# Performance work log

Hardware: AMD Instinct MI355X
Metric: run time of the kernel (lower is better)

Reference implementation:

```python
import math
import jax, jax.numpy as jnp
import numpy as np

L, NH, DF = 4, 4, 32  # num_layers, num_heads, head_dim (H=128)
EPS = 1e-5


def ln(x, g, b):
    m = x.mean(-1, keepdims=True)
    v = ((x - m) ** 2).mean(-1, keepdims=True)
    return (x - m) * jax.lax.rsqrt(v + EPS) * g + b


def mha(x, w_in, b_in, w_out, b_out):
    # torch nn.MultiheadAttention self-attention, batch_first, no mask
    B, S, H = x.shape
    q, k, v = jnp.split(x @ w_in + b_in, 3, axis=-1)
    q = q.reshape(B, S, NH, DF)
    k = k.reshape(B, S, NH, DF)
    v = v.reshape(B, S, NH, DF)
    s = jnp.einsum('bqhd,bkhd->bhqk', q, k) / math.sqrt(DF)
    a = jax.nn.softmax(s, axis=-1)
    o = jnp.einsum('bhqk,bkhd->bqhd', a, v).reshape(B, S, H)
    return o @ w_out + b_out


def _forward(X_k, time_embed, step_embed, W_tr, b_tr, W_in, b_in, g_in, be_in,
             W_e, b_e, aw, ab, ow, ob, tng, tnb, f1w, f1b, f2w, f2b, fng, fnb,
             Wq, Wk, Wv, Wo, bo, Wem, bem, Wea, bea, e1w, e1b, e2w, e2b,
             gng, gnb, eng, enb, W_out, b_out, k_index, edge_index):
    B, N, T1, Cin = X_k.shape
    H = W_in.shape[1]
    # --- precompute_graph: self-loops + structural edge features ---
    loop = jnp.arange(N, dtype=edge_index.dtype)
    ei = jnp.concatenate([edge_index, jnp.stack([loop, loop])], axis=1)
    dst, src = ei[0], ei[1]
    E = ei.shape[1]
    deg = jnp.zeros((N,), jnp.float32).at[dst].add(1.0)
    deg_max = jnp.maximum(deg.max(), 1.0)
    edge_w = 1.0 / jnp.maximum(deg[dst], 1.0)
    feat = jnp.stack([edge_w, deg[src] / deg_max, deg[dst] / deg_max], axis=1)  # [E,3]
    # --- input embedding ---
    t_emb = time_embed  # [T1, te] (lookup of arange(T1) = whole table)
    X = jnp.concatenate(
        [X_k, jnp.broadcast_to(t_emb[None, None], (B, N, T1, t_emb.shape[-1]))], axis=-1)
    h = ln(X @ W_in + b_in, g_in, be_in)
    h = h + step_embed[k_index][:, None, None, :]
    e = feat @ W_e + b_e                       # [E, de]
    t_re = t_emb @ W_tr + b_tr                 # [T1, H]
    BT = B * T1
    for l in range(L):
        # temporal attention over T1
        h_flat = h.reshape(B * N, T1, H)
        attn_out = mha(h_flat, aw[l], ab[l], ow[l], ob[l])
        h = ln(h + attn_out.reshape(B, N, T1, H), tng[l], tnb[l])
        ffn = jax.nn.gelu(h @ f1w[l] + f1b[l], approximate=False) @ f2w[l] + f2b[l]
        h = ln(h + ffn, fng[l], fnb[l])
        h = h + t_re[None, None]
        # DiGress GT sparse graph block over N
        h_BT = h.transpose(0, 2, 1, 3).reshape(BT, N, H)
        Q = (h_BT @ Wq[l]).reshape(BT, N, NH, DF)
        K = (h_BT @ Wk[l]).reshape(BT, N, NH, DF)
        V = (h_BT @ Wv[l]).reshape(BT, N, NH, DF)
        scores = (Q[:, dst] * K[:, src]).sum(-1) / math.sqrt(DF)  # [BT,E,NH]
        scores = scores * (e @ Wem[l] + bem[l] + 1.0) + (e @ Wea[l] + bea[l])
        s_max = jax.lax.stop_gradient(scores.max(axis=1, keepdims=True))
        exp_s = jnp.exp(scores - s_max)
        denom = jnp.zeros((BT, N, NH), exp_s.dtype).at[:, dst, :].add(exp_s)
        attn = exp_s / (denom[:, dst, :] + 1e-9)
        agg = (attn[..., None] * V[:, src]).reshape(BT, E, H)
        out = jnp.zeros((BT, N, H), h.dtype).at[:, dst, :].add(agg)
        h_BT = h_BT + out @ Wo[l] + bo[l]
        h_mean = jax.lax.stop_gradient(h_BT).mean(0)               # [N,H]
        e_in = jnp.concatenate([h_mean[dst], h_mean[src], e], axis=-1)
        e_mlp = jax.nn.gelu(e_in @ e1w[l] + e1b[l], approximate=False) @ e2w[l] + e2b[l]
        e = ln(e + e_mlp, eng[l], enb[l])
        h = ln(h_BT.reshape(B, T1, N, H).transpose(0, 2, 1, 3), gng[l], gnb[l])
    return jax.nn.softmax(h @ W_out + b_out, axis=-1)


def setup_inputs() -> dict:
    key = jax.random.key(0)
    B, N, T1 = 2, 2000, 12
    sd, cc, te, H, de, nh = 4, 2, 16, 128, 16, 4
    Cin = (1 + cc) * sd  # 12
    E0, max_steps = 32000, 1024
    ks = iter(jax.random.split(key, 60))
    def rn(*shape, s=0.05):
        return jax.random.normal(next(ks), shape, jnp.float32) * s
    z = lambda *s: jnp.zeros(s, jnp.float32)
    o = lambda *s: jnp.ones(s, jnp.float32)
    return dict(
        X_k=jax.random.normal(next(ks), (B, N, T1, Cin), jnp.float32),
        time_embed=rn(T1, te), step_embed=rn(max_steps, H),
        W_tr=rn(te, H), b_tr=z(H),
        W_in=rn(Cin + te, H), b_in=z(H), g_in=o(H), be_in=z(H),
        W_e=rn(3, de), b_e=z(de),
        aw=rn(L, H, 3 * H), ab=z(L, 3 * H), ow=rn(L, H, H), ob=z(L, H),
        tng=o(L, H), tnb=z(L, H),
        f1w=rn(L, H, 2 * H), f1b=z(L, 2 * H), f2w=rn(L, 2 * H, H), f2b=z(L, H),
        fng=o(L, H), fnb=z(L, H),
        Wq=rn(L, H, H), Wk=rn(L, H, H), Wv=rn(L, H, H),
        Wo=rn(L, H, H), bo=z(L, H),
        Wem=rn(L, de, nh), bem=z(L, nh), Wea=rn(L, de, nh), bea=z(L, nh),
        e1w=rn(L, 2 * H + de, 4 * de), e1b=z(L, 4 * de),
        e2w=rn(L, 4 * de, de), e2b=z(L, de),
        gng=o(L, H), gnb=z(L, H), eng=o(L, de), enb=z(L, de),
        W_out=rn(H, sd), b_out=z(sd),
        k_index=jax.random.randint(next(ks), (B,), 0, max_steps),
        edge_index=jax.random.randint(next(ks), (2, E0), 0, N),
    )


def reference(X_k, time_embed, step_embed, W_tr, b_tr, W_in, b_in, g_in, be_in,
              W_e, b_e, aw, ab, ow, ob, tng, tnb, f1w, f1b, f2w, f2b, fng, fnb,
              Wq, Wk, Wv, Wo, bo, Wem, bem, Wea, bea, e1w, e1b, e2w, e2b,
              gng, gnb, eng, enb, W_out, b_out, k_index, edge_index):
    return _forward(X_k, time_embed, step_embed, W_tr, b_tr, W_in, b_in, g_in, be_in,
                    W_e, b_e, aw, ab, ow, ob, tng, tnb, f1w, f1b, f2w, f2b, fng, fnb,
                    Wq, Wk, Wv, Wo, bo, Wem, bem, Wea, bea, e1w, e1b, e2w, e2b,
                    gng, gnb, eng, enb, W_out, b_out, k_index, edge_index)
```

## Files before the change

kernel.cpp:

```cpp
#include <hip/hip_runtime.h>
#include <math.h>

#define NN 2000
#define T1C 12
#define BBC 2
#define HHC 128
#define NHD 4
#define DFD 32
#define LLC 4
#define DEC 16
#define TEC 16
#define CINC 12
#define E0C 32000
#define EEC 34000
#define BTC 24
#define MROWS 48000
#define EPSLN 1e-5f
#define SCALEQK 0.17677669529663687f

typedef __attribute__((ext_vector_type(8))) short short8;
typedef __attribute__((ext_vector_type(4))) float f32x4;


__device__ __forceinline__ unsigned short f2b(float f)
{
    unsigned u = __float_as_uint(f);
    return (unsigned short)((u + 0x7FFF + ((u >> 16) & 1)) >> 16);
}

__device__ __forceinline__ float b2f(unsigned short h)
{
    return __uint_as_float(((unsigned)h) << 16);
}


__global__ __launch_bounds__(256) void convwp_k(const float* __restrict__ W, unsigned short* __restrict__ Bp,
                                                int LN_, int K, int N, int noff, int Ntot)
{
    int idx = blockIdx.x * blockDim.x + threadIdx.x;
    int total = LN_ * K * N;
    if (idx >= total) return;
    int l = idx / (K * N);
    int r = idx - l * (K * N);
    int k = r / N;
    int n = r - k * N + noff;
    size_t off = (size_t)l * K * Ntot +
                 ((size_t)((n >> 4) * (K >> 5) + (k >> 5)) << 9) +
                 (((k >> 3) & 3) << 7) + ((n & 15) << 3) + (k & 7);
    Bp[off] = f2b(W[idx]);
}

__global__ __launch_bounds__(256) void convw12_k(const float* __restrict__ e1w, unsigned short* __restrict__ W12P)
{
    int idx = blockIdx.x * blockDim.x + threadIdx.x;
    if (idx >= LLC * 128 * 128) return;
    int l = idx >> 14;
    int r = idx & 16383;
    int c = r >> 7, k = r & 127;
    int sk = (c < 64) ? k : k + 128;
    int sc = c & 63;
    W12P[idx] = f2b(e1w[((size_t)l * 272 + sk) * 64 + sc]);
}

__global__ __launch_bounds__(256) void convwoT_k(const float* __restrict__ Wo, unsigned short* __restrict__ WoT)
{
    int idx = blockIdx.x * blockDim.x + threadIdx.x;
    if (idx >= LLC * 128 * 128) return;
    int l = idx >> 14;
    int r = idx & 16383;
    int c = r >> 7, k = r & 127;
    WoT[idx] = f2b(Wo[((size_t)l * 128 + k) * 128 + c]);
}


template<int K, int EPI, int OUTM>
__global__ __launch_bounds__(256) void gemm2_k(
    const unsigned short* __restrict__ A, const unsigned short* __restrict__ Bp,
    const float* __restrict__ bias, float* __restrict__ C, unsigned short* __restrict__ Cb,
    const float* __restrict__ res, const float* __restrict__ gam, const float* __restrict__ bet,
    const float* __restrict__ trep,
    int M, int Ntot)
{
    __shared__ unsigned short A_s[128 * 16 * 8];
    __shared__ float red2[2][128][2];

    int tid = threadIdx.x;
    int w = tid >> 6, lane = tid & 63;
    int wr = w & 1, wc = w >> 1;
    int quad = lane >> 4, lr = lane & 15;

    const unsigned short* abase = A + (size_t)blockIdx.x * 128 * K;
    int ntg0 = blockIdx.y * 8 + wc * 4;

    f32x4 acc[4][4];
#pragma unroll
    for (int mt = 0; mt < 4; mt++)
#pragma unroll
        for (int nt = 0; nt < 4; nt++) acc[mt][nt] = (f32x4){0.f, 0.f, 0.f, 0.f};

#pragma unroll
    for (int kb = 0; kb < K; kb += 128) {
        if (kb) __syncthreads();
#pragma unroll
        for (int j = 0; j < 8; j++) {
            int s = j * 256 + tid;
            int row = s >> 4, ks = s & 15;
            int ko = ks ^ (row & 15);
            uint4 d = *(const uint4*)(abase + (size_t)row * K + kb + ko * 8);
            *(uint4*)(A_s + s * 8) = d;
        }
        __syncthreads();
#pragma unroll
        for (int k0 = 0; k0 < 128; k0 += 32) {
            short8 af[4], bf[4];
#pragma unroll
            for (int mt = 0; mt < 4; mt++) {
                int row_l = wr * 64 + mt * 16 + lr;
                int koct = (k0 >> 3) + quad;
                int slot = row_l * 16 + (koct ^ lr);
                af[mt] = *(const short8*)(A_s + slot * 8);
            }
#pragma unroll
            for (int nt = 0; nt < 4; nt++) {
                size_t off = ((size_t)(ntg0 + nt) * (K >> 5) + ((kb + k0) >> 5)) * 512 + lane * 8;
                bf[nt] = *(const short8*)(Bp + off);
            }
#pragma unroll
            for (int mt = 0; mt < 4; mt++)
#pragma unroll
                for (int nt = 0; nt < 4; nt++)
                    acc[mt][nt] = __builtin_amdgcn_mfma_f32_16x16x32_bf16(af[mt], bf[nt], acc[mt][nt], 0, 0, 0);
        }
    }

    int rbase = blockIdx.x * 128 + wr * 64;
    int cbase = blockIdx.y * 128 + wc * 64;

    if constexpr (EPI != 3 && EPI != 4 && EPI != 5) {
#pragma unroll
        for (int mt = 0; mt < 4; mt++) {
#pragma unroll
            for (int nt = 0; nt < 4; nt++) {
                int colg = cbase + nt * 16 + lr;
                float bv = bias ? bias[colg] : 0.f;
#pragma unroll
                for (int i = 0; i < 4; i++) {
                    int row = rbase + mt * 16 + quad * 4 + i;
                    float x = acc[mt][nt][i] + bv;
                    if constexpr (EPI == 1) x = 0.5f * x * (1.f + erff(x * 0.70710678118654752f));
                    if constexpr (EPI == 2) x = res[(size_t)row * Ntot + colg] + x;
                    if constexpr (OUTM & 1) C[(size_t)row * Ntot + colg] = x;
                    if constexpr (OUTM & 4)
                        Cb[(size_t)blockIdx.y * M * 128 + (size_t)row * 128 + (wc * 64 + nt * 16 + lr)] = f2b(x);
                    else if constexpr (OUTM & 2)
                        Cb[(size_t)row * Ntot + colg] = f2b(x);
                }
            }
        }
    } else {
        float s[4][4], s2l[4][4];
#pragma unroll
        for (int mt = 0; mt < 4; mt++)
#pragma unroll
            for (int i = 0; i < 4; i++) { s[mt][i] = 0.f; s2l[mt][i] = 0.f; }
#pragma unroll
        for (int mt = 0; mt < 4; mt++) {
#pragma unroll
            for (int nt = 0; nt < 4; nt++) {
                int colg = cbase + nt * 16 + lr;
                float bv = bias[colg];
#pragma unroll
                for (int i = 0; i < 4; i++) {
                    int row = rbase + mt * 16 + quad * 4 + i;
                    float x = acc[mt][nt][i] + bv + res[(size_t)row * 128 + colg];
                    acc[mt][nt][i] = x;
                    s[mt][i] += x;
                    s2l[mt][i] += x * x;
                }
            }
        }
#pragma unroll
        for (int m = 1; m < 16; m <<= 1) {
#pragma unroll
            for (int mt = 0; mt < 4; mt++)
#pragma unroll
                for (int i = 0; i < 4; i++) {
                    s[mt][i]  += __shfl_xor(s[mt][i], m, 64);
                    s2l[mt][i] += __shfl_xor(s2l[mt][i], m, 64);
                }
        }
        if (lr == 0) {
#pragma unroll
            for (int mt = 0; mt < 4; mt++)
#pragma unroll
                for (int i = 0; i < 4; i++) {
                    int rl = wr * 64 + mt * 16 + quad * 4 + i;
                    red2[wc][rl][0] = s[mt][i];
                    red2[wc][rl][1] = s2l[mt][i];
                }
        }
        __syncthreads();
#pragma unroll
        for (int mt = 0; mt < 4; mt++) {
#pragma unroll
            for (int i = 0; i < 4; i++) {
                int rl = wr * 64 + mt * 16 + quad * 4 + i;
                float st  = red2[0][rl][0] + red2[1][rl][0];
                float s2t = red2[0][rl][1] + red2[1][rl][1];
                float mu = st * (1.f / 128.f);
                float rstd = rsqrtf(s2t * (1.f / 128.f) - mu * mu + EPSLN);
                int row = rbase + mt * 16 + quad * 4 + i;
                if constexpr (EPI == 4) {
                    int t = row % T1C;
                    int bn = row / T1C;
                    int b = bn / NN;
                    int n = bn - b * NN;
                    size_t rowp = (size_t)(b * T1C + t) * NN + n;
                    const float* trow = trep + t * HHC;
#pragma unroll
                    for (int nt = 0; nt < 4; nt++) {
                        int colg = cbase + nt * 16 + lr;
                        float y = (acc[mt][nt][i] - mu) * rstd * gam[colg] + bet[colg] + trow[colg];
                        C[rowp * 128 + colg] = y;
                        Cb[rowp * 128 + colg] = f2b(y);
                    }
                } else if constexpr (EPI == 5) {
                    int bt = row / NN, n = row - bt * NN;
                    int b = bt / T1C, t = bt - b * T1C;
                    size_t rowp = ((size_t)(b * NN + n)) * T1C + t;
#pragma unroll
                    for (int nt = 0; nt < 4; nt++) {
                        int colg = cbase + nt * 16 + lr;
                        float y = (acc[mt][nt][i] - mu) * rstd * gam[colg] + bet[colg];
                        C[rowp * 128 + colg] = y;
                        Cb[rowp * 128 + colg] = f2b(y);
                    }
                } else {
#pragma unroll
                    for (int nt = 0; nt < 4; nt++) {
                        int colg = cbase + nt * 16 + lr;
                        float y = (acc[mt][nt][i] - mu) * rstd * gam[colg] + bet[colg];
                        if constexpr (OUTM & 1) C[(size_t)row * 128 + colg] = y;
                        if constexpr (OUTM & 2) Cb[(size_t)row * 128 + colg] = f2b(y);
                    }
                }
            }
        }
    }
}

template<int K, int EPI, int OUTM>
static void run_gemm2(const unsigned short* A, const unsigned short* Bp, const float* bias,
                      float* C, unsigned short* Cb, const float* res, const float* g, const float* be,
                      const float* trep, int M, int Ntot, hipStream_t stream)
{
    dim3 grid(M / 128, Ntot / 128);
    gemm2_k<K, EPI, OUTM><<<grid, 256, 0, stream>>>(A, Bp, bias, C, Cb, res, g, be, trep, M, Ntot);
}


__global__ __launch_bounds__(256) void offn_k(
    const unsigned short* __restrict__ A,
    const unsigned short* __restrict__ Wp,
    const float* __restrict__ ob_l,
    const float* __restrict__ resh,
    const float* __restrict__ tng_l, const float* __restrict__ tnb_l,
    const unsigned short* __restrict__ F1p,
    const unsigned short* __restrict__ F2p,
    const float* __restrict__ f1b_l, const float* __restrict__ f2b_l,
    const float* __restrict__ fng_l, const float* __restrict__ fnb_l,
    const float* __restrict__ trep,
    const unsigned short* __restrict__ Wqkv,
    float* __restrict__ C,
    unsigned short* __restrict__ Qc, unsigned short* __restrict__ Kc, unsigned short* __restrict__ Vc)
{
    __shared__ unsigned short A_s[32 * 16 * 8];
    __shared__ unsigned short M_s[32 * 16 * 8];
    __shared__ float red2[2][32][2];

    int tid = threadIdx.x;
    int w = tid >> 6, lane = tid & 63;
    int wr = w & 1, wc = w >> 1;
    int quad = lane >> 4, lr = lane & 15;

    const unsigned short* abase = A + (size_t)blockIdx.x * 32 * 128;

#pragma unroll
    for (int j = 0; j < 2; j++) {
        int s = j * 256 + tid;
        int row = s >> 4, ks = s & 15;
        int ko = ks ^ (row & 15);
        uint4 d = *(const uint4*)(abase + (size_t)row * 128 + ko * 8);
        *(uint4*)(A_s + s * 8) = d;
    }
    __syncthreads();

    f32x4 wacc[4];
#pragma unroll
    for (int nt = 0; nt < 4; nt++) wacc[nt] = (f32x4){0.f, 0.f, 0.f, 0.f};
#pragma unroll
    for (int k0 = 0; k0 < 128; k0 += 32) {
        int row_l = wr * 16 + lr;
        int koct = (k0 >> 3) + quad;
        int slot = row_l * 16 + (koct ^ lr);
        short8 af = *(const short8*)(A_s + slot * 8);
        short8 bf[4];
#pragma unroll
        for (int nt = 0; nt < 4; nt++) {
            size_t off = ((size_t)(wc * 4 + nt) * 4 + (k0 >> 5)) * 512 + lane * 8;
            bf[nt] = *(const short8*)(Wp + off);
        }
#pragma unroll
        for (int nt = 0; nt < 4; nt++)
            wacc[nt] = __builtin_amdgcn_mfma_f32_16x16x32_bf16(af, bf[nt], wacc[nt], 0, 0, 0);
    }

    int rbase = blockIdx.x * 32 + wr * 16;
    int cbase = wc * 64;

    float yv[4][4];
    {
        float s1[4], s2v[4];
#pragma unroll
        for (int i = 0; i < 4; i++) { s1[i] = 0.f; s2v[i] = 0.f; }
#pragma unroll
        for (int nt = 0; nt < 4; nt++) {
            int colg = cbase + nt * 16 + lr;
            float bv = ob_l[colg];
#pragma unroll
            for (int i = 0; i < 4; i++) {
                int row = rbase + quad * 4 + i;
                float x = wacc[nt][i] + bv + resh[(size_t)row * 128 + colg];
                yv[nt][i] = x;
                s1[i] += x;
                s2v[i] += x * x;
            }
        }
#pragma unroll
        for (int m = 1; m < 16; m <<= 1) {
#pragma unroll
            for (int i = 0; i < 4; i++) {
                s1[i]  += __shfl_xor(s1[i], m, 64);
                s2v[i] += __shfl_xor(s2v[i], m, 64);
            }
        }
        if (lr == 0) {
#pragma unroll
            for (int i = 0; i < 4; i++) {
                int rl = wr * 16 + quad * 4 + i;
                red2[wc][rl][0] = s1[i];
                red2[wc][rl][1] = s2v[i];
            }
        }
        __syncthreads();
#pragma unroll
        for (int i = 0; i < 4; i++) {
            int rl = wr * 16 + quad * 4 + i;
            float st  = red2[0][rl][0] + red2[1][rl][0];
            float s2t = red2[0][rl][1] + red2[1][rl][1];
            float mu = st * (1.f / 128.f);
            float rstd = rsqrtf(s2t * (1.f / 128.f) - mu * mu + EPSLN);
            int row = wr * 16 + quad * 4 + i;
#pragma unroll
            for (int nt = 0; nt < 4; nt++) {
                int col = cbase + nt * 16 + lr;
                float y = (yv[nt][i] - mu) * rstd * tng_l[col] + tnb_l[col];
                yv[nt][i] = y;
                int cchunk = col >> 3, celem = col & 7;
                int ks = cchunk ^ (row & 15);
                A_s[(row * 16 + ks) * 8 + celem] = f2b(y);
            }
        }
    }
    __syncthreads();

    f32x4 facc[4];
#pragma unroll
    for (int nt = 0; nt < 4; nt++) facc[nt] = (f32x4){0.f, 0.f, 0.f, 0.f};

#pragma unroll
    for (int half = 0; half < 2; half++) {
        f32x4 macc[4];
#pragma unroll
        for (int nt = 0; nt < 4; nt++) macc[nt] = (f32x4){0.f, 0.f, 0.f, 0.f};
#pragma unroll
        for (int k0 = 0; k0 < 128; k0 += 32) {
            int row_l = wr * 16 + lr;
            int koct = (k0 >> 3) + quad;
            int slot = row_l * 16 + (koct ^ lr);
            short8 af = *(const short8*)(A_s + slot * 8);
            short8 bf[4];
#pragma unroll
            for (int nt = 0; nt < 4; nt++) {
                size_t off = ((size_t)(half * 8 + wc * 4 + nt) * 4 + (k0 >> 5)) * 512 + lane * 8;
                bf[nt] = *(const short8*)(F1p + off);
            }
#pragma unroll
            for (int nt = 0; nt < 4; nt++)
                macc[nt] = __builtin_amdgcn_mfma_f32_16x16x32_bf16(af, bf[nt], macc[nt], 0, 0, 0);
        }
        if (half) __syncthreads();
#pragma unroll
        for (int nt = 0; nt < 4; nt++) {
            int col = wc * 64 + nt * 16 + lr;
            float bv = f1b_l[half * 128 + col];
            int cchunk = col >> 3, celem = col & 7;
#pragma unroll
            for (int i = 0; i < 4; i++) {
                int row = wr * 16 + quad * 4 + i;
                float x = macc[nt][i] + bv;
                x = 0.5f * x * (1.f + erff(x * 0.70710678118654752f));
                int ks = cchunk ^ (row & 15);
                M_s[(row * 16 + ks) * 8 + celem] = f2b(x);
            }
        }
        __syncthreads();
#pragma unroll
        for (int k0 = 0; k0 < 128; k0 += 32) {
            int row_l = wr * 16 + lr;
            int koct = (k0 >> 3) + quad;
            int slot = row_l * 16 + (koct ^ lr);
            short8 af = *(const short8*)(M_s + slot * 8);
            short8 bf[4];
#pragma unroll
            for (int nt = 0; nt < 4; nt++) {
                size_t off = ((size_t)(wc * 4 + nt) * 8 + ((half * 128 + k0) >> 5)) * 512 + lane * 8;
                bf[nt] = *(const short8*)(F2p + off);
            }
#pragma unroll
            for (int nt = 0; nt < 4; nt++)
                facc[nt] = __builtin_amdgcn_mfma_f32_16x16x32_bf16(af, bf[nt], facc[nt], 0, 0, 0);
        }
    }

    float s[4], s2l[4];
#pragma unroll
    for (int i = 0; i < 4; i++) { s[i] = 0.f; s2l[i] = 0.f; }
#pragma unroll
    for (int nt = 0; nt < 4; nt++) {
        int colg = cbase + nt * 16 + lr;
        float bv = f2b_l[colg];
#pragma unroll
        for (int i = 0; i < 4; i++) {
            float x = facc[nt][i] + bv + yv[nt][i];
            facc[nt][i] = x;
            s[i] += x;
            s2l[i] += x * x;
        }
    }
#pragma unroll
    for (int m = 1; m < 16; m <<= 1) {
#pragma unroll
        for (int i = 0; i < 4; i++) {
            s[i]  += __shfl_xor(s[i], m, 64);
            s2l[i] += __shfl_xor(s2l[i], m, 64);
        }
    }
    if (lr == 0) {
#pragma unroll
        for (int i = 0; i < 4; i++) {
            int rl = wr * 16 + quad * 4 + i;
            red2[wc][rl][0] = s[i];
            red2[wc][rl][1] = s2l[i];
        }
    }
    __syncthreads();
    size_t rowp4[4];
#pragma unroll
    for (int i = 0; i < 4; i++) {
        int rl = wr * 16 + quad * 4 + i;
        float st  = red2[0][rl][0] + red2[1][rl][0];
        float s2t = red2[0][rl][1] + red2[1][rl][1];
        float mu = st * (1.f / 128.f);
        float rstd = rsqrtf(s2t * (1.f / 128.f) - mu * mu + EPSLN);
        int row = rbase + quad * 4 + i;
        int t = row % T1C;
        int bn = row / T1C;
        int b = bn / NN;
        int n = bn - b * NN;
        size_t rowp = (size_t)(b * T1C + t) * NN + n;
        rowp4[i] = rowp;
        const float* trow = trep + t * HHC;
        int rloc = wr * 16 + quad * 4 + i;
#pragma unroll
        for (int nt = 0; nt < 4; nt++) {
            int colg = cbase + nt * 16 + lr;
            float y = (facc[nt][i] - mu) * rstd * fng_l[colg] + fnb_l[colg] + trow[colg];
            C[rowp * 128 + colg] = y;
            int cchunk = colg >> 3, celem = colg & 7;
            int ks = cchunk ^ (rloc & 15);
            A_s[(rloc * 16 + ks) * 8 + celem] = f2b(y);
        }
    }
    __syncthreads();

#pragma unroll
    for (int g3 = 0; g3 < 3; g3++) {
        f32x4 qacc[4];
#pragma unroll
        for (int nt = 0; nt < 4; nt++) qacc[nt] = (f32x4){0.f, 0.f, 0.f, 0.f};
#pragma unroll
        for (int k0 = 0; k0 < 128; k0 += 32) {
            int row_l = wr * 16 + lr;
            int koct = (k0 >> 3) + quad;
            int slot = row_l * 16 + (koct ^ lr);
            short8 af = *(const short8*)(A_s + slot * 8);
            short8 bf[4];
#pragma unroll
            for (int nt = 0; nt < 4; nt++) {
                size_t off = ((size_t)(wc * 12 + g3 * 4 + nt) * 4 + (k0 >> 5)) * 512 + lane * 8;
                bf[nt] = *(const short8*)(Wqkv + off);
            }
#pragma unroll
            for (int nt = 0; nt < 4; nt++)
                qacc[nt] = __builtin_amdgcn_mfma_f32_16x16x32_bf16(af, bf[nt], qacc[nt], 0, 0, 0);
        }
#pragma unroll
        for (int nt = 0; nt < 4; nt++) {
            int colg = wc * 192 + (g3 * 4 + nt) * 16 + lr;
            unsigned short* dstbuf;
            int col;
            if (colg < 128)      { dstbuf = Qc; col = colg; }
            else if (colg < 256) { dstbuf = Kc; col = colg - 128; }
            else                 { dstbuf = Vc; col = colg - 256; }
#pragma unroll
            for (int i = 0; i < 4; i++)
                dstbuf[rowp4[i] * 128 + col] = f2b(qacc[nt][i]);
        }
    }
}


template<int NT>
__global__ __launch_bounds__(256) void gemm_mfma_k(
    const unsigned short* __restrict__ A, const unsigned short* __restrict__ WT,
    float* __restrict__ C, int M, int K)
{
    const int Nc = NT * 32;
    int tid = threadIdx.x;
    int w = tid >> 6, lane = tid & 63;
    int wr = w & 1, wc = w >> 1;
    int r0 = blockIdx.x * 32 + wr * 16;
    int c0 = wc * NT * 16;
    int lr = lane & 15;
    int kq = (lane >> 4) * 8;
    int arow = r0 + lr; if (arow >= M) arow = M - 1;
    const unsigned short* ap = A + (size_t)arow * K + kq;
    const unsigned short* wp = WT + (size_t)(c0 + lr) * K + kq;

    f32x4 acc[NT];
#pragma unroll
    for (int t = 0; t < NT; t++) acc[t] = (f32x4){0.f, 0.f, 0.f, 0.f};

    for (int k0 = 0; k0 < K; k0 += 32) {
        short8 a = *(const short8*)(ap + k0);
#pragma unroll
        for (int t = 0; t < NT; t++) {
            short8 b = *(const short8*)(wp + (size_t)t * 16 * K + k0);
            acc[t] = __builtin_amdgcn_mfma_f32_16x16x32_bf16(a, b, acc[t], 0, 0, 0);
        }
    }

    int orow0 = r0 + (lane >> 4) * 4;
#pragma unroll
    for (int t = 0; t < NT; t++) {
        int col = c0 + t * 16 + lr;
#pragma unroll
        for (int i = 0; i < 4; i++) {
            int row = orow0 + i;
            if (row < M) C[(size_t)row * Nc + col] = acc[t][i];
        }
    }
}

__global__ __launch_bounds__(256) void gemm_hm_k(
    const unsigned short* __restrict__ A, const unsigned short* __restrict__ WT,
    const float* __restrict__ mA, const float* __restrict__ bo,
    unsigned short* __restrict__ hmb, int M, int K)
{
    const int NT = 4;
    int tid = threadIdx.x;
    int w = tid >> 6, lane = tid & 63;
    int wr = w & 1, wc = w >> 1;
    int r0 = blockIdx.x * 32 + wr * 16;
    int c0 = wc * NT * 16;
    int lr = lane & 15;
    int kq = (lane >> 4) * 8;
    int arow = r0 + lr; if (arow >= M) arow = M - 1;
    const unsigned short* ap = A + (size_t)arow * K + kq;
    const unsigned short* wp = WT + (size_t)(c0 + lr) * K + kq;

    f32x4 acc[NT];
#pragma unroll
    for (int t = 0; t < NT; t++) acc[t] = (f32x4){0.f, 0.f, 0.f, 0.f};

    for (int k0 = 0; k0 < K; k0 += 32) {
        short8 a = *(const short8*)(ap + k0);
#pragma unroll
        for (int t = 0; t < NT; t++) {
            short8 b = *(const short8*)(wp + (size_t)t * 16 * K + k0);
            acc[t] = __builtin_amdgcn_mfma_f32_16x16x32_bf16(a, b, acc[t], 0, 0, 0);
        }
    }

    int orow0 = r0 + (lane >> 4) * 4;
#pragma unroll
    for (int t = 0; t < NT; t++) {
        int col = c0 + t * 16 + lr;
#pragma unroll
        for (int i = 0; i < 4; i++) {
            int row = orow0 + i;
            if (row < M) {
                float x = acc[t][i] + mA[(size_t)row * 128 + col] + bo[col];
                hmb[(size_t)row * 128 + col] = f2b(x);
            }
        }
    }
}


__global__ __launch_bounds__(256) void emlp_k(const float* __restrict__ P12,
                                              const int* __restrict__ dst, const int* __restrict__ src,
                                              const float* __restrict__ e1wE, const float* __restrict__ e1b_l,
                                              const float* __restrict__ e2w_l, const float* __restrict__ e2b_l,
                                              const float* __restrict__ g, const float* __restrict__ be,
                                              float* __restrict__ e)
{
    __shared__ float tl[4][64];
    int wv = threadIdx.x >> 6, l = threadIdx.x & 63;
    int r = blockIdx.x * 4 + wv;
    int d = dst[r], s = src[r];
    const float* ep = e + (size_t)r * DEC;
    float t = P12[(size_t)d * 128 + l] + P12[(size_t)s * 128 + 64 + l] + e1b_l[l];
#pragma unroll
    for (int k = 0; k < DEC; k++) t += ep[k] * e1wE[k * 64 + l];
    t = 0.5f * t * (1.f + erff(t * 0.70710678118654752f));
    tl[wv][l] = t;
    __syncthreads();
    int c = l & 15, kq = l >> 4;
    float p = 0.f;
#pragma unroll
    for (int j = 0; j < 16; j++) p += tl[wv][kq * 16 + j] * e2w_l[(kq * 16 + j) * 16 + c];
    p += __shfl_xor(p, 16, 64);
    p += __shfl_xor(p, 32, 64);
    float x = p + e2b_l[c] + ep[c];
    float s1 = x, s2 = x * x;
#pragma unroll
    for (int m = 1; m < 16; m <<= 1) {
        s1 += __shfl_xor(s1, m, 64);
        s2 += __shfl_xor(s2, m, 64);
    }
    float mu = s1 * (1.f / 16.f);
    float rstd = rsqrtf(s2 * (1.f / 16.f) - mu * mu + EPSLN);
    float y = (x - mu) * rstd * g[c] + be[c];
    if (l < 16) e[(size_t)r * DEC + c] = y;
}


__global__ __launch_bounds__(256) void zero_deg_k(int* __restrict__ degi)
{
    int i = blockIdx.x * blockDim.x + threadIdx.x;
    if (i < NN) degi[i] = 0;
}

__global__ __launch_bounds__(256) void build_edges_k(const int* __restrict__ eidx,
                                                     int* __restrict__ dst, int* __restrict__ src,
                                                     int* __restrict__ degi)
{
    int e = blockIdx.x * blockDim.x + threadIdx.x;
    if (e >= EEC) return;
    int d, s;
    if (e < E0C) { d = eidx[e]; s = eidx[E0C + e]; }
    else { d = e - E0C; s = e - E0C; }
    dst[e] = d;
    src[e] = s;
    atomicAdd(&degi[d], 1);
}

__global__ __launch_bounds__(256) void scan_k(const int* __restrict__ degi, int* __restrict__ rowptr,
                                              int* __restrict__ cursor, float* __restrict__ degmaxf)
{
    __shared__ int ssum[256];
    __shared__ int smx[256];
    int tid = threadIdx.x;
    int vals[8];
    int s = 0, mx = 0;
    int base = tid * 8;
#pragma unroll
    for (int j = 0; j < 8; j++) {
        int idx = base + j;
        int v = (idx < NN) ? degi[idx] : 0;
        vals[j] = v; s += v; mx = max(mx, v);
    }
    ssum[tid] = s; smx[tid] = mx;
    __syncthreads();
    for (int off = 1; off < 256; off <<= 1) {
        int t = (tid >= off) ? ssum[tid - off] : 0;
        __syncthreads();
        ssum[tid] += t;
        __syncthreads();
    }
    for (int off = 128; off > 0; off >>= 1) {
        if (tid < off) smx[tid] = max(smx[tid], smx[tid + off]);
        __syncthreads();
    }
    if (tid == 0) *degmaxf = fmaxf((float)smx[0], 1.f);
    int running = ssum[tid] - s;
#pragma unroll
    for (int j = 0; j < 8; j++) {
        int idx = base + j;
        if (idx < NN) { rowptr[idx] = running; cursor[idx] = running; running += vals[j]; }
    }
    if (tid == 255) rowptr[NN] = ssum[255];
}

__global__ __launch_bounds__(256) void feat_k(const int* __restrict__ dst, const int* __restrict__ src,
                                              const int* __restrict__ degi, const float* __restrict__ degmaxf,
                                              int* __restrict__ cursor, int* __restrict__ srcCSR,
                                              int* __restrict__ epos,
                                              const float* __restrict__ We, const float* __restrict__ bE,
                                              float* __restrict__ e)
{
    int ei = blockIdx.x * blockDim.x + threadIdx.x;
    if (ei >= EEC) return;
    int d = dst[ei], s = src[ei];
    int pos = atomicAdd(&cursor[d], 1);
    srcCSR[pos] = s;
    epos[ei] = pos;
    float dm = *degmaxf;
    float degd = (float)degi[d], degs = (float)degi[s];
    float f0 = 1.f / fmaxf(degd, 1.f);
    float f1 = degs / dm, f2 = degd / dm;
#pragma unroll
    for (int c = 0; c < DEC; c++)
        e[ei * DEC + c] = bE[c] + f0 * We[c] + f1 * We[DEC + c] + f2 * We[2 * DEC + c];
}


__global__ __launch_bounds__(256) void embed_k(const float* __restrict__ Xk, const float* __restrict__ temb,
                                               const float* __restrict__ Win, const float* __restrict__ bin,
                                               const float* __restrict__ g, const float* __restrict__ be,
                                               const float* __restrict__ stepemb, const int* __restrict__ kidx,
                                               float* __restrict__ h, unsigned short* __restrict__ hb)
{
    int row = blockIdx.x * 4 + (threadIdx.x >> 6);
    int l = threadIdx.x & 63;
    int t = row % T1C;
    int bn = row / T1C;
    int b = bn / NN;
    const float* xk = Xk + (size_t)row * CINC;
    const float* tp = temb + t * TEC;
    float acc0 = bin[l], acc1 = bin[l + 64];
#pragma unroll
    for (int k = 0; k < CINC; k++) {
        float xv = xk[k];
        acc0 += xv * Win[k * HHC + l];
        acc1 += xv * Win[k * HHC + l + 64];
    }
#pragma unroll
    for (int k = 0; k < TEC; k++) {
        float xv = tp[k];
        acc0 += xv * Win[(CINC + k) * HHC + l];
        acc1 += xv * Win[(CINC + k) * HHC + l + 64];
    }
    float s = acc0 + acc1, s2 = acc0 * acc0 + acc1 * acc1;
#pragma unroll
    for (int m = 32; m >= 1; m >>= 1) {
        s  += __shfl_xor(s, m, 64);
        s2 += __shfl_xor(s2, m, 64);
    }
    float mu = s * (1.f / 128.f);
    float rstd = rsqrtf(s2 * (1.f / 128.f) - mu * mu + EPSLN);
    const float* se = stepemb + (size_t)kidx[b] * HHC;
    float v0 = (acc0 - mu) * rstd * g[l] + be[l] + se[l];
    float v1 = (acc1 - mu) * rstd * g[l + 64] + be[l + 64] + se[l + 64];
    size_t ob = (size_t)row * HHC;
    h[ob + l] = v0;
    h[ob + l + 64] = v1;
    hb[ob + l] = f2b(v0);
    hb[ob + l + 64] = f2b(v1);
}

__global__ __launch_bounds__(128) void tre_k(const float* __restrict__ temb, const float* __restrict__ Wtr,
                                             const float* __restrict__ btr, float* __restrict__ tre)
{
    int t = blockIdx.x, c = threadIdx.x;
    float acc = btr[c];
#pragma unroll
    for (int k = 0; k < TEC; k++) acc += temb[t * TEC + k] * Wtr[k * HHC + c];
    tre[t * HHC + c] = acc;
}


__global__ __launch_bounds__(128) void temporal_attn_k(const unsigned short* __restrict__ qkvb,
                                                       unsigned short* __restrict__ outb)
{
    int bn = blockIdx.x;
    __shared__ unsigned short qkv_s[T1C][408];
    __shared__ float s[NHD][T1C][T1C];
    int tid = threadIdx.x;
    int hh = tid >> 5, lane = tid & 31;
    const unsigned short* base = qkvb + (size_t)bn * T1C * 384;
    for (int cIdx = tid; cIdx < 576; cIdx += 128) {
        uint4 d = *(const uint4*)(base + cIdx * 8);
        int t = cIdx / 48;
        int c0 = (cIdx - t * 48) * 8;
        *(uint4*)(&qkv_s[t][c0]) = d;
    }
    __syncthreads();
    for (int idx = lane; idx < T1C * T1C; idx += 32) {
        int tq = idx / T1C, tk = idx - tq * T1C;
        const unsigned* qp = (const unsigned*)&qkv_s[tq][hh * 32];
        const unsigned* kp = (const unsigned*)&qkv_s[tk][128 + hh * 32];
        float acc = 0.f;
#pragma unroll
        for (int d = 0; d < 16; d++) {
            unsigned a = qp[d], b = kp[d];
            acc += __uint_as_float(a << 16) * __uint_as_float(b << 16);
            acc += __uint_as_float(a & 0xFFFF0000u) * __uint_as_float(b & 0xFFFF0000u);
        }
        s[hh][tq][tk] = acc * SCALEQK;
    }
    __syncthreads();
    if (tid < NHD * T1C) {
        int h2 = tid / T1C, tq = tid - h2 * T1C;
        float mx = -1e30f;
#pragma unroll
        for (int j = 0; j < T1C; j++) mx = fmaxf(mx, s[h2][tq][j]);
        float sum = 0.f;
#pragma unroll
        for (int j = 0; j < T1C; j++) { float ex = __expf(s[h2][tq][j] - mx); s[h2][tq][j] = ex; sum += ex; }
        float inv = 1.f / sum;
#pragma unroll
        for (int j = 0; j < T1C; j++) s[h2][tq][j] *= inv;
    }
    __syncthreads();
    int oc = hh * 32 + lane;
#pragma unroll
    for (int t = 0; t < T1C; t++) {
        float acc = 0.f;
#pragma unroll
        for (int tk = 0; tk < T1C; tk++) acc += s[hh][t][tk] * b2f(qkv_s[tk][256 + oc]);
        outb[((size_t)bn * T1C + t) * HHC + oc] = f2b(acc);
    }
}


__global__ __launch_bounds__(256) void emea_k(const float* __restrict__ e, const int* __restrict__ epos,
                                              const float* __restrict__ Wem, const float* __restrict__ bem,
                                              const float* __restrict__ Wea, const float* __restrict__ bea,
                                              float* __restrict__ ec)
{
    int r = blockIdx.x * blockDim.x + threadIdx.x;
    if (r >= EEC) return;
    float ev[DEC];
#pragma unroll
    for (int k = 0; k < DEC; k++) ev[k] = e[r * DEC + k];
    int pos = epos[r];
#pragma unroll
    for (int hh = 0; hh < NHD; hh++) {
        float a = bem[hh], b2 = bea[hh];
#pragma unroll
        for (int k = 0; k < DEC; k++) { a += ev[k] * Wem[k * NHD + hh]; b2 += ev[k] * Wea[k * NHD + hh]; }
        ec[(size_t)pos * 8 + hh * 2]     = (a + 1.f) * SCALEQK;
        ec[(size_t)pos * 8 + hh * 2 + 1] = b2;
    }
}

__global__ __launch_bounds__(256) void sagg_k(const unsigned short* __restrict__ Q,
                                              const unsigned short* __restrict__ K,
                                              const unsigned short* __restrict__ V,
                                              const int* __restrict__ rowptr, const int* __restrict__ srcCSR,
                                              const float* __restrict__ ec, unsigned short* __restrict__ outb)
{
    int wv = threadIdx.x >> 6;
    int lane = threadIdx.x & 63;
    int blk = blockIdx.x;
    int bt = blk % BTC;
    int n  = (blk / BTC) * 4 + wv;
    int cg = lane & 15;
    int es = lane >> 4;
    int hh = cg >> 2;
    size_t base = (size_t)bt * NN;
    uint4 qd = *(const uint4*)(Q + (base + n) * HHC + cg * 8);
    unsigned qv[4] = {qd.x, qd.y, qd.z, qd.w};
    float q[8];
#pragma unroll
    for (int jj = 0; jj < 4; jj++) {
        q[2 * jj]     = __uint_as_float(qv[jj] << 16);
        q[2 * jj + 1] = __uint_as_float(qv[jj] & 0xFFFF0000u);
    }
    int s0 = rowptr[n], s1 = rowptr[n + 1];
    float acc[8];
#pragma unroll
    for (int j = 0; j < 8; j++) acc[j] = 0.f;
    float den = 0.f;
    for (int i = s0 + es; i < s1; i += 4) {
        int sn = srcCSR[i];
        uint4 kd = *(const uint4*)(K + (base + sn) * HHC + cg * 8);
        uint4 vd = *(const uint4*)(V + (base + sn) * HHC + cg * 8);
        float2 c2 = *(const float2*)(ec + (size_t)i * 8 + hh * 2);
        unsigned kv[4] = {kd.x, kd.y, kd.z, kd.w};
        float p = 0.f;
#pragma unroll
        for (int jj = 0; jj < 4; jj++) {
            p += q[2 * jj]     * __uint_as_float(kv[jj] << 16);
            p += q[2 * jj + 1] * __uint_as_float(kv[jj] & 0xFFFF0000u);
        }
        p += __shfl_xor(p, 1, 64);
        p += __shfl_xor(p, 2, 64);
        float w = __expf(p * c2.x + c2.y);
        unsigned vv[4] = {vd.x, vd.y, vd.z, vd.w};
#pragma unroll
        for (int jj = 0; jj < 4; jj++) {
            acc[2 * jj]     += w * __uint_as_float(vv[jj] << 16);
            acc[2 * jj + 1] += w * __uint_as_float(vv[jj] & 0xFFFF0000u);
        }
        den += w;
    }
#pragma unroll
    for (int j = 0; j < 8; j++) {
        acc[j] += __shfl_xor(acc[j], 16, 64);
        acc[j] += __shfl_xor(acc[j], 32, 64);
    }
    den += __shfl_xor(den, 16, 64);
    den += __shfl_xor(den, 32, 64);
    if (es == 0) {
        float inv = den + 1e-9f;
        unsigned short r[8];
#pragma unroll
        for (int j = 0; j < 8; j++) r[j] = f2b(acc[j] / inv);
        *(uint4*)(outb + (base + n) * HHC + cg * 8) = *(uint4*)r;
    }
}

__global__ __launch_bounds__(128) void hmean2_k(const float* __restrict__ hBT,
                                                const unsigned short* __restrict__ aggb,
                                                float* __restrict__ mA, unsigned short* __restrict__ mBb)
{
    int n = blockIdx.x, c = threadIdx.x;
    float sA = 0.f, sB = 0.f;
#pragma unroll
    for (int bt = 0; bt < BTC; bt++) {
        size_t off = ((size_t)bt * NN + n) * HHC + c;
        sA += hBT[off];
        sB += b2f(aggb[off]);
    }
    mA[n * HHC + c] = sA * (1.f / BTC);
    mBb[n * HHC + c] = f2b(sB * (1.f / BTC));
}


__global__ __launch_bounds__(256) void out_k(const float* __restrict__ h, const float* __restrict__ Wout,
                                             const float* __restrict__ bout, float* __restrict__ out)
{
    int row = blockIdx.x * 4 + (threadIdx.x >> 6);
    int lane = threadIdx.x & 63;
    const float* hp = h + (size_t)row * HHC;
    float x0 = hp[lane], x1 = hp[lane + 64];
    float w00 = Wout[lane * 4 + 0], w01 = Wout[lane * 4 + 1];
    float w02 = Wout[lane * 4 + 2], w03 = Wout[lane * 4 + 3];
    float w10 = Wout[(lane + 64) * 4 + 0], w11 = Wout[(lane + 64) * 4 + 1];
    float w12 = Wout[(lane + 64) * 4 + 2], w13 = Wout[(lane + 64) * 4 + 3];
    float p0 = x0 * w00 + x1 * w10;
    float p1 = x0 * w01 + x1 * w11;
    float p2 = x0 * w02 + x1 * w12;
    float p3 = x0 * w03 + x1 * w13;
#pragma unroll
    for (int m = 32; m >= 1; m >>= 1) {
        p0 += __shfl_xor(p0, m, 64);
        p1 += __shfl_xor(p1, m, 64);
        p2 += __shfl_xor(p2, m, 64);
        p3 += __shfl_xor(p3, m, 64);
    }
    if (lane == 0) {
        float l0 = p0 + bout[0], l1 = p1 + bout[1], l2 = p2 + bout[2], l3 = p3 + bout[3];
        float mx = fmaxf(fmaxf(l0, l1), fmaxf(l2, l3));
        float e0 = __expf(l0 - mx), e1 = __expf(l1 - mx), e2 = __expf(l2 - mx), e3 = __expf(l3 - mx);
        float inv = 1.f / (e0 + e1 + e2 + e3);
        float4 o = {e0 * inv, e1 * inv, e2 * inv, e3 * inv};
        *(float4*)(out + (size_t)row * 4) = o;
    }
}


extern "C" void kernel_launch(void* const* d_in, const int* in_sizes, int n_in,
                              void* d_out, int out_size, void* d_ws, size_t ws_size,
                              hipStream_t stream)
{
    const float* Xk      = (const float*)d_in[0];
    const float* temb    = (const float*)d_in[1];
    const float* stepemb = (const float*)d_in[2];
    const float* Wtr     = (const float*)d_in[3];
    const float* btr     = (const float*)d_in[4];
    const float* Win     = (const float*)d_in[5];
    const float* bin     = (const float*)d_in[6];
    const float* gin     = (const float*)d_in[7];
    const float* bein    = (const float*)d_in[8];
    const float* We      = (const float*)d_in[9];
    const float* bE      = (const float*)d_in[10];
    const float* aw      = (const float*)d_in[11];
    const float* ab      = (const float*)d_in[12];
    const float* ow      = (const float*)d_in[13];
    const float* ob      = (const float*)d_in[14];
    const float* tng     = (const float*)d_in[15];
    const float* tnb     = (const float*)d_in[16];
    const float* f1w     = (const float*)d_in[17];
    const float* f1b     = (const float*)d_in[18];
    const float* f2w     = (const float*)d_in[19];
    const float* f2b_    = (const float*)d_in[20];
    const float* fng     = (const float*)d_in[21];
    const float* fnb     = (const float*)d_in[22];
    const float* Wq      = (const float*)d_in[23];
    const float* Wk      = (const float*)d_in[24];
    const float* Wv      = (const float*)d_in[25];
    const float* Wo      = (const float*)d_in[26];
    const float* bo      = (const float*)d_in[27];
    const float* Wem     = (const float*)d_in[28];
    const float* bem     = (const float*)d_in[29];
    const float* Wea     = (const float*)d_in[30];
    const float* bea     = (const float*)d_in[31];
    const float* e1w     = (const float*)d_in[32];
    const float* e1b     = (const float*)d_in[33];
    const float* e2w     = (const float*)d_in[34];
    const float* e2b     = (const float*)d_in[35];
    const float* gng     = (const float*)d_in[36];
    const float* gnb     = (const float*)d_in[37];
    const float* eng     = (const float*)d_in[38];
    const float* enb     = (const float*)d_in[39];
    const float* Wout    = (const float*)d_in[40];
    const float* bout    = (const float*)d_in[41];
    const int*   kidx    = (const int*)d_in[42];
    const int*   eidx    = (const int*)d_in[43];
    float* outp = (float*)d_out;

    char* wsp = (char*)d_ws;
    auto alloc = [&](size_t nbytes) -> void* {
        void* p = (void*)wsp;
        wsp += (nbytes + 255) & ~(size_t)255;
        return p;
    };
    float* h     = (float*)alloc((size_t)MROWS * HHC * 4);
    unsigned short* hb = (unsigned short*)alloc((size_t)MROWS * HHC * 2);
    float* hBT   = (float*)alloc((size_t)MROWS * HHC * 4);
    unsigned short* hBTb = (unsigned short*)alloc((size_t)MROWS * HHC * 2);
    float* bufC  = (float*)alloc((size_t)MROWS * 384 * 4);
    unsigned short* bufDb = (unsigned short*)alloc((size_t)MROWS * HHC * 2);
    float* ebuf  = (float*)alloc((size_t)EEC * DEC * 4);
    float* ec    = (float*)alloc((size_t)EEC * NHD * 2 * 4);
    float* P12   = (float*)alloc((size_t)NN * HHC * 4);
    float* mA    = (float*)alloc((size_t)NN * HHC * 4);
    unsigned short* mBb = (unsigned short*)alloc((size_t)NN * HHC * 2);
    unsigned short* hmb = (unsigned short*)alloc((size_t)NN * HHC * 2);
    float* tre   = (float*)alloc((size_t)T1C * HHC * 4);
    float* degmaxf = (float*)alloc(4);
    int* degi   = (int*)alloc((size_t)NN * 4);
    int* dst    = (int*)alloc((size_t)EEC * 4);
    int* srcA   = (int*)alloc((size_t)EEC * 4);
    int* srcCSR = (int*)alloc((size_t)EEC * 4);
    int* epos   = (int*)alloc((size_t)EEC * 4);
    int* rowptr = (int*)alloc((size_t)(NN + 1) * 4);
    int* cursor = (int*)alloc((size_t)NN * 4);
    unsigned short* awP   = (unsigned short*)alloc((size_t)LLC * 384 * 128 * 2);
    unsigned short* owP   = (unsigned short*)alloc((size_t)LLC * 128 * 128 * 2);
    unsigned short* f1P   = (unsigned short*)alloc((size_t)LLC * 256 * 128 * 2);
    unsigned short* f2P   = (unsigned short*)alloc((size_t)LLC * 128 * 256 * 2);
    unsigned short* WqkvP = (unsigned short*)alloc((size_t)LLC * 384 * 128 * 2);
    unsigned short* WoP   = (unsigned short*)alloc((size_t)LLC * 128 * 128 * 2);
    unsigned short* WoT   = (unsigned short*)alloc((size_t)LLC * 128 * 128 * 2);
    unsigned short* W12P  = (unsigned short*)alloc((size_t)LLC * 128 * 128 * 2);

    unsigned short* bufCb = (unsigned short*)bufC;
    unsigned short* Qc    = (unsigned short*)bufC;
    unsigned short* Kc    = Qc + (size_t)MROWS * HHC;
    unsigned short* Vc    = Kc + (size_t)MROWS * HHC;

    {
        auto cwp = [&](const float* W, unsigned short* Bp, int K, int N, int noff, int Ntot) {
            int total = LLC * K * N;
            convwp_k<<<(total + 255) / 256, 256, 0, stream>>>(W, Bp, LLC, K, N, noff, Ntot);
        };
        cwp(aw,  awP, 128, 384, 0, 384);
        cwp(ow,  owP, 128, 128, 0, 128);
        cwp(f1w, f1P, 128, 256, 0, 256);
        cwp(f2w, f2P, 256, 128, 0, 128);
        cwp(Wq,  WqkvP, 128, 128, 0,   384);
        cwp(Wk,  WqkvP, 128, 128, 128, 384);
        cwp(Wv,  WqkvP, 128, 128, 256, 384);
        cwp(Wo,  WoP, 128, 128, 0, 128);
        convwoT_k<<<(LLC * 128 * 128 + 255) / 256, 256, 0, stream>>>(Wo, WoT);
        convw12_k<<<(LLC * 128 * 128 + 255) / 256, 256, 0, stream>>>(e1w, W12P);
    }

    zero_deg_k<<<(NN + 255) / 256, 256, 0, stream>>>(degi);
    build_edges_k<<<(EEC + 255) / 256, 256, 0, stream>>>(eidx, dst, srcA, degi);
    scan_k<<<1, 256, 0, stream>>>(degi, rowptr, cursor, degmaxf);
    feat_k<<<(EEC + 255) / 256, 256, 0, stream>>>(dst, srcA, degi, degmaxf, cursor, srcCSR, epos, We, bE, ebuf);

    embed_k<<<MROWS / 4, 256, 0, stream>>>(Xk, temb, Win, bin, gin, bein, stepemb, kidx, h, hb);
    tre_k<<<T1C, 128, 0, stream>>>(temb, Wtr, btr, tre);

    for (int l = 0; l < LLC; l++) {
        const unsigned short* awP_l   = awP   + (size_t)l * 384 * 128;
        const unsigned short* owP_l   = owP   + (size_t)l * 128 * 128;
        const unsigned short* f1P_l   = f1P   + (size_t)l * 256 * 128;
        const unsigned short* f2P_l   = f2P   + (size_t)l * 128 * 256;
        const unsigned short* WqkvP_l = WqkvP + (size_t)l * 384 * 128;
        const unsigned short* WoP_l   = WoP   + (size_t)l * 128 * 128;
        const unsigned short* WoT_l   = WoT   + (size_t)l * 128 * 128;
        const unsigned short* W12P_l  = W12P  + (size_t)l * 128 * 128;
        const float* ab_l  = ab  + (size_t)l * 3 * HHC;
        const float* ob_l  = ob  + (size_t)l * HHC;
        const float* tng_l = tng + (size_t)l * HHC;
        const float* tnb_l = tnb + (size_t)l * HHC;
        const float* f1b_l = f1b + (size_t)l * 256;
        const float* f2b_l = f2b_ + (size_t)l * HHC;
        const float* fng_l = fng + (size_t)l * HHC;
        const float* fnb_l = fnb + (size_t)l * HHC;
        const float* bo_l  = bo  + (size_t)l * HHC;
        const float* Wem_l = Wem + (size_t)l * DEC * NHD;
        const float* bem_l = bem + (size_t)l * NHD;
        const float* Wea_l = Wea + (size_t)l * DEC * NHD;
        const float* bea_l = bea + (size_t)l * NHD;
        const float* e1wE_l = e1w + ((size_t)l * 272 + 256) * 64;
        const float* e1b_l = e1b + (size_t)l * 64;
        const float* e2w_l = e2w + (size_t)l * 64 * DEC;
        const float* e2b_l = e2b + (size_t)l * DEC;
        const float* gng_l = gng + (size_t)l * HHC;
        const float* gnb_l = gnb + (size_t)l * HHC;
        const float* eng_l = eng + (size_t)l * DEC;
        const float* enb_l = enb + (size_t)l * DEC;

        run_gemm2<128, 0, 2>(hb, awP_l, ab_l, nullptr, bufCb, nullptr, nullptr, nullptr, nullptr, MROWS, 384, stream);
        temporal_attn_k<<<BBC * NN, 128, 0, stream>>>(bufCb, bufDb);
        offn_k<<<MROWS / 32, 256, 0, stream>>>(bufDb, owP_l, ob_l, h, tng_l, tnb_l,
                                               f1P_l, f2P_l, f1b_l, f2b_l, fng_l, fnb_l,
                                               tre, WqkvP_l, hBT, Qc, Kc, Vc);
        emea_k<<<(EEC + 255) / 256, 256, 0, stream>>>(ebuf, epos, Wem_l, bem_l, Wea_l, bea_l, ec);
        sagg_k<<<BTC * (NN / 4), 256, 0, stream>>>(Qc, Kc, Vc, rowptr, srcCSR, ec, bufDb);
        hmean2_k<<<NN, 128, 0, stream>>>(hBT, bufDb, mA, mBb);
        run_gemm2<128, 5, 3>(bufDb, WoP_l, bo_l, h, hb, hBT, gng_l, gnb_l, nullptr, MROWS, 128, stream);
        gemm_hm_k<<<(NN + 31) / 32, 256, 0, stream>>>(mBb, WoT_l, mA, bo_l, hmb, NN, 128);
        gemm_mfma_k<4><<<(NN + 31) / 32, 256, 0, stream>>>(hmb, W12P_l, P12, NN, 128);
        emlp_k<<<EEC / 4, 256, 0, stream>>>(P12, dst, srcA, e1wE_l, e1b_l, e2w_l, e2b_l, eng_l, enb_l, ebuf);
    }

    out_k<<<MROWS / 4, 256, 0, stream>>>(h, Wout, bout, outp);
}
```

Baseline: 972.8 us.

## Fuse node-mean reduction with two chained node GEMMs into one kernel

Replaces the hmean2, gemm_hm and gemm_mfma kernels with a single hm12_k kernel. It computes the per-node means over B*T, runs the Wo GEMM with bias and residual, and then the W12 GEMM, keeping intermediates in swizzled shared memory. This removes two launches and the global round trips for mA, mBb and hmb. In exchange, the mean reduction over the large hBT and aggregation buffers now runs on only about 63 blocks instead of 2000, which may limit memory bandwidth.

```diff
diff --git a/kernel.cpp b/kernel.cpp
--- a/kernel.cpp
+++ b/kernel.cpp
@@ -531,89 +531,103 @@
 }
 
 
-template<int NT>
-__global__ __launch_bounds__(256) void gemm_mfma_k(
-    const unsigned short* __restrict__ A, const unsigned short* __restrict__ WT,
-    float* __restrict__ C, int M, int K)
-{
-    const int Nc = NT * 32;
+__global__ __launch_bounds__(256) void hm12_k(
+    const float* __restrict__ hBT, const unsigned short* __restrict__ aggb,
+    const unsigned short* __restrict__ WoT,
+    const float* __restrict__ bo,
+    const unsigned short* __restrict__ W12,
+    float* __restrict__ P12)
+{
+    __shared__ float mA_s[32][128];
+    __shared__ unsigned short A_s[32 * 16 * 8];
+
     int tid = threadIdx.x;
+    int n0 = blockIdx.x * 32;
+
+#pragma unroll 1
+    for (int it = 0; it < 16; it++) {
+        int rloc = it * 2 + (tid >> 7);
+        int c = tid & 127;
+        int n = n0 + rloc; if (n >= NN) n = NN - 1;
+        float sA = 0.f, sB = 0.f;
+#pragma unroll
+        for (int bt = 0; bt < BTC; bt++) {
+            size_t off = ((size_t)bt * NN + n) * HHC + c;
+            sA += hBT[off];
+            sB += b2f(aggb[off]);
+        }
+        mA_s[rloc][c] = sA * (1.f / BTC);
+        int cchunk = c >> 3, celem = c & 7;
+        int ks = cchunk ^ (rloc & 15);
+        A_s[(rloc * 16 + ks) * 8 + celem] = f2b(sB * (1.f / BTC));
+    }
+    __syncthreads();
+
     int w = tid >> 6, lane = tid & 63;
     int wr = w & 1, wc = w >> 1;
-    int r0 = blockIdx.x * 32 + wr * 16;
-    int c0 = wc * NT * 16;
-    int lr = lane & 15;
-    int kq = (lane >> 4) * 8;
-    int arow = r0 + lr; if (arow >= M) arow = M - 1;
-    const unsigned short* ap = A + (size_t)arow * K + kq;
-    const unsigned short* wp = WT + (size_t)(c0 + lr) * K + kq;
-
-    f32x4 acc[NT];
-#pragma unroll
-    for (int t = 0; t < NT; t++) acc[t] = (f32x4){0.f, 0.f, 0.f, 0.f};
-
-    for (int k0 = 0; k0 < K; k0 += 32) {
-        short8 a = *(const short8*)(ap + k0);
-#pragma unroll
-        for (int t = 0; t < NT; t++) {
-            short8 b = *(const short8*)(wp + (size_t)t * 16 * K + k0);
-            acc[t] = __builtin_amdgcn_mfma_f32_16x16x32_bf16(a, b, acc[t], 0, 0, 0);
-        }
-    }
-
-    int orow0 = r0 + (lane >> 4) * 4;
-#pragma unroll
-    for (int t = 0; t < NT; t++) {
-        int col = c0 + t * 16 + lr;
+    int lr = lane & 15, quad = lane >> 4;
+    int kq = quad * 8;
+
+    f32x4 acc[4];
+#pragma unroll
+    for (int nt = 0; nt < 4; nt++) acc[nt] = (f32x4){0.f, 0.f, 0.f, 0.f};
+#pragma unroll
+    for (int k0 = 0; k0 < 128; k0 += 32) {
+        int row_l = wr * 16 + lr;
+        int koct = (k0 >> 3) + quad;
+        int slot = row_l * 16 + (koct ^ lr);
+        short8 af = *(const short8*)(A_s + slot * 8);
+        short8 bf[4];
+#pragma unroll
+        for (int nt = 0; nt < 4; nt++) {
+            int col = wc * 64 + nt * 16 + lr;
+            bf[nt] = *(const short8*)(WoT + (size_t)col * 128 + kq + k0);
+        }
+#pragma unroll
+        for (int nt = 0; nt < 4; nt++)
+            acc[nt] = __builtin_amdgcn_mfma_f32_16x16x32_bf16(af, bf[nt], acc[nt], 0, 0, 0);
+    }
+    __syncthreads();
+#pragma unroll
+    for (int nt = 0; nt < 4; nt++) {
+        int col = wc * 64 + nt * 16 + lr;
+        int cchunk = col >> 3, celem = col & 7;
 #pragma unroll
         for (int i = 0; i < 4; i++) {
-            int row = orow0 + i;
-            if (row < M) C[(size_t)row * Nc + col] = acc[t][i];
-        }
-    }
-}
-
-__global__ __launch_bounds__(256) void gemm_hm_k(
-    const unsigned short* __restrict__ A, const unsigned short* __restrict__ WT,
-    const float* __restrict__ mA, const float* __restrict__ bo,
-    unsigned short* __restrict__ hmb, int M, int K)
-{
-    const int NT = 4;
-    int tid = threadIdx.x;
-    int w = tid >> 6, lane = tid & 63;
-    int wr = w & 1, wc = w >> 1;
-    int r0 = blockIdx.x * 32 + wr * 16;
-    int c0 = wc * NT * 16;
-    int lr = lane & 15;
-    int kq = (lane >> 4) * 8;
-    int arow = r0 + lr; if (arow >= M) arow = M - 1;
-    const unsigned short* ap = A + (size_t)arow * K + kq;
-    const unsigned short* wp = WT + (size_t)(c0 + lr) * K + kq;
-
-    f32x4 acc[NT];
-#pragma unroll
-    for (int t = 0; t < NT; t++) acc[t] = (f32x4){0.f, 0.f, 0.f, 0.f};
-
-    for (int k0 = 0; k0 < K; k0 += 32) {
-        short8 a = *(const short8*)(ap + k0);
-#pragma unroll
-        for (int t = 0; t < NT; t++) {
-            short8 b = *(const short8*)(wp + (size_t)t * 16 * K + k0);
-            acc[t] = __builtin_amdgcn_mfma_f32_16x16x32_bf16(a, b, acc[t], 0, 0, 0);
-        }
-    }
-
-    int orow0 = r0 + (lane >> 4) * 4;
-#pragma unroll
-    for (int t = 0; t < NT; t++) {
-        int col = c0 + t * 16 + lr;
+            int rloc = wr * 16 + quad * 4 + i;
+            float x = acc[nt][i] + mA_s[rloc][col] + bo[col];
+            int ks = cchunk ^ (rloc & 15);
+            A_s[(rloc * 16 + ks) * 8 + celem] = f2b(x);
+        }
+    }
+    __syncthreads();
+
+    f32x4 acc2[4];
+#pragma unroll
+    for (int nt = 0; nt < 4; nt++) acc2[nt] = (f32x4){0.f, 0.f, 0.f, 0.f};
+#pragma unroll
+    for (int k0 = 0; k0 < 128; k0 += 32) {
+        int row_l = wr * 16 + lr;
+        int koct = (k0 >> 3) + quad;
+        int slot = row_l * 16 + (koct ^ lr);
+        short8 af = *(const short8*)(A_s + slot * 8);
+        short8 bf[4];
+#pragma unroll
+        for (int nt = 0; nt < 4; nt++) {
+            int col = wc * 64 + nt * 16 + lr;
+            bf[nt] = *(const short8*)(W12 + (size_t)col * 128 + kq + k0);
+        }
+#pragma unroll
+        for (int nt = 0; nt < 4; nt++)
+            acc2[nt] = __builtin_amdgcn_mfma_f32_16x16x32_bf16(af, bf[nt], acc2[nt], 0, 0, 0);
+    }
+#pragma unroll
+    for (int nt = 0; nt < 4; nt++) {
+        int col = wc * 64 + nt * 16 + lr;
 #pragma unroll
         for (int i = 0; i < 4; i++) {
-            int row = orow0 + i;
-            if (row < M) {
-                float x = acc[t][i] + mA[(size_t)row * 128 + col] + bo[col];
-                hmb[(size_t)row * 128 + col] = f2b(x);
-            }
+            int row = n0 + wr * 16 + quad * 4 + i;
+            if (row < NN) P12[(size_t)row * 128 + col] = acc2[nt][i];
         }
     }
 }
@@ -932,22 +946,6 @@
         for (int j = 0; j < 8; j++) r[j] = f2b(acc[j] / inv);
         *(uint4*)(outb + (base + n) * HHC + cg * 8) = *(uint4*)r;
     }
-}
-
-__global__ __launch_bounds__(128) void hmean2_k(const float* __restrict__ hBT,
-                                                const unsigned short* __restrict__ aggb,
-                                                float* __restrict__ mA, unsigned short* __restrict__ mBb)
-{
-    int n = blockIdx.x, c = threadIdx.x;
-    float sA = 0.f, sB = 0.f;
-#pragma unroll
-    for (int bt = 0; bt < BTC; bt++) {
-        size_t off = ((size_t)bt * NN + n) * HHC + c;
-        sA += hBT[off];
-        sB += b2f(aggb[off]);
-    }
-    mA[n * HHC + c] = sA * (1.f / BTC);
-    mBb[n * HHC + c] = f2b(sB * (1.f / BTC));
 }
 
 
@@ -1043,15 +1041,11 @@
     float* h     = (float*)alloc((size_t)MROWS * HHC * 4);
     unsigned short* hb = (unsigned short*)alloc((size_t)MROWS * HHC * 2);
     float* hBT   = (float*)alloc((size_t)MROWS * HHC * 4);
-    unsigned short* hBTb = (unsigned short*)alloc((size_t)MROWS * HHC * 2);
     float* bufC  = (float*)alloc((size_t)MROWS * 384 * 4);
     unsigned short* bufDb = (unsigned short*)alloc((size_t)MROWS * HHC * 2);
     float* ebuf  = (float*)alloc((size_t)EEC * DEC * 4);
     float* ec    = (float*)alloc((size_t)EEC * NHD * 2 * 4);
     float* P12   = (float*)alloc((size_t)NN * HHC * 4);
-    float* mA    = (float*)alloc((size_t)NN * HHC * 4);
-    unsigned short* mBb = (unsigned short*)alloc((size_t)NN * HHC * 2);
-    unsigned short* hmb = (unsigned short*)alloc((size_t)NN * HHC * 2);
     float* tre   = (float*)alloc((size_t)T1C * HHC * 4);
     float* degmaxf = (float*)alloc(4);
     int* degi   = (int*)alloc((size_t)NN * 4);
@@ -1138,10 +1132,8 @@
                                                tre, WqkvP_l, hBT, Qc, Kc, Vc);
         emea_k<<<(EEC + 255) / 256, 256, 0, stream>>>(ebuf, epos, Wem_l, bem_l, Wea_l, bea_l, ec);
         sagg_k<<<BTC * (NN / 4), 256, 0, stream>>>(Qc, Kc, Vc, rowptr, srcCSR, ec, bufDb);
-        hmean2_k<<<NN, 128, 0, stream>>>(hBT, bufDb, mA, mBb);
+        hm12_k<<<(NN + 31) / 32, 256, 0, stream>>>(hBT, bufDb, WoT_l, bo_l, W12P_l, P12);
         run_gemm2<128, 5, 3>(bufDb, WoP_l, bo_l, h, hb, hBT, gng_l, gnb_l, nullptr, MROWS, 128, stream);
-        gemm_hm_k<<<(NN + 31) / 32, 256, 0, stream>>>(mBb, WoT_l, mA, bo_l, hmb, NN, 128);
-        gemm_mfma_k<4><<<(NN + 31) / 32, 256, 0, stream>>>(hmb, W12P_l, P12, NN, 128);
         emlp_k<<<EEC / 4, 256, 0, stream>>>(P12, dst, srcA, e1wE_l, e1b_l, e2w_l, e2b_l, eng_l, enb_l, ebuf);
     }
 
```

Result: slower. 1.138 ms (+17.0%).
